# Optimization experiments

Hardware: AMD Instinct MI355X
Metric: run time of the kernel (lower is better)

The kernel has to match this reference:

```python
import jax, jax.numpy as jnp
import numpy as np

# Haar step along H (axis 1 of a (B,H,W) image): average / abs-diff of row pairs.
def _haar_y(img):
    odd, even = img[:, 0::2], img[:, 1::2]
    return (odd + even) / 2.0, jnp.abs(odd - even)

# Haar step along W (axis 2). In the original torch code this is done via
# permute + flip + Y-transform + permute + flip-back; the two flips act on the
# untouched H axis and cancel exactly, so the math reduces to pairing along W.
def _haar_x(img):
    odd, even = img[:, :, 0::2], img[:, :, 1::2]
    return (odd + even) / 2.0, jnp.abs(odd - even)

def _dwt2(img):  # (B,H,W) -> LL, LH, HL, HH each (B,H/2,W/2)
    L, H = _haar_y(img)
    LL, LH = _haar_x(L)
    HL, HH = _haar_x(H)
    return LL, LH, HL, HH

def setup_inputs() -> dict:
    key = jax.random.key(0)
    x = jax.random.uniform(key, (32, 3, 512, 512), dtype=jnp.float32)
    return {"x": x}

def reference(x):
    r, g, b = x[:, 0], x[:, 1], x[:, 2]
    # Level 1
    r1 = _dwt2(r); g1 = _dwt2(g); b1 = _dwt2(b)
    t1 = jnp.stack([*r1, *g1, *b1], axis=1)  # (B,12,H/2,W/2)
    # Level 2 (recursion on LL of each channel)
    r2 = _dwt2(r1[0]); g2 = _dwt2(g1[0]); b2 = _dwt2(b1[0])
    t2 = jnp.stack([*r2, *g2, *b2], axis=1)
    # Level 3
    r3 = _dwt2(r2[0]); g3 = _dwt2(g2[0]); b3 = _dwt2(b2[0])
    t3 = jnp.stack([*r3, *g3, *b3], axis=1)
    # Level 4 -- faithfully reproduces the original bug: the blue-channel
    # level-4 bands are computed from wavelet_L4/H4 left over from the green
    # channel, so b4 == g4.
    r4 = _dwt2(r3[0]); g4 = _dwt2(g3[0]); b4 = g4
    t4 = jnp.stack([*r4, *g4, *b4], axis=1)
    return (t1, t2, t3, t4)
```

## Files before the change

### kernel.cpp

```cpp
#include <hip/hip_runtime.h>

__global__ __launch_bounds__(256) void dwt_level_kernel(
    const float* __restrict__ src, float* __restrict__ dst,
    int W,
    int h, int shift,
    long src_b_stride, long src_c_stride,
    int nC, int dup)
{
    int pid = blockIdx.x * blockDim.x + threadIdx.x;
    int npix = h << shift;
    if (pid >= npix) return;

    int plane = blockIdx.y;
    int b = plane / nC;
    int c = plane - b * nC;

    int jw = pid & ((1 << shift) - 1);
    int i  = pid >> shift;

    const float* sp = src + (long)b * src_b_stride + (long)c * src_c_stride;
    const float4 r0 = *((const float4*)(sp + (long)(2 * i)     * W) + jw);
    const float4 r1 = *((const float4*)(sp + (long)(2 * i + 1) * W) + jw);

    float L00 = (r0.x + r1.x) * 0.5f;
    float L01 = (r0.y + r1.y) * 0.5f;
    float H00 = fabsf(r0.x - r1.x);
    float H01 = fabsf(r0.y - r1.y);
    float L10 = (r0.z + r1.z) * 0.5f;
    float L11 = (r0.w + r1.w) * 0.5f;
    float H10 = fabsf(r0.z - r1.z);
    float H11 = fabsf(r0.w - r1.w);

    float2 ll = make_float2((L00 + L01) * 0.5f, (L10 + L11) * 0.5f);
    float2 lh = make_float2(fabsf(L00 - L01), fabsf(L10 - L11));
    float2 hl = make_float2((H00 + H01) * 0.5f, (H10 + H11) * 0.5f);
    float2 hh = make_float2(fabsf(H00 - H01), fabsf(H10 - H11));

    int w = 2 << shift;
    long hw = (long)h * w;
    float* dp = dst + (long)(b * 12 + 4 * c) * hw + (long)i * w + 2 * jw;

    *(float2*)(dp + 0 * hw) = ll;
    *(float2*)(dp + 1 * hw) = lh;
    *(float2*)(dp + 2 * hw) = hl;
    *(float2*)(dp + 3 * hw) = hh;

    if (dup && c == nC - 1) {
        float* dp2 = dp + 4 * hw;
        *(float2*)(dp2 + 0 * hw) = ll;
        *(float2*)(dp2 + 1 * hw) = lh;
        *(float2*)(dp2 + 2 * hw) = hl;
        *(float2*)(dp2 + 3 * hw) = hh;
    }
}

extern "C" void kernel_launch(void* const* d_in, const int* in_sizes, int n_in,
                              void* d_out, int out_size, void* d_ws, size_t ws_size,
                              hipStream_t stream) {
    const float* x = (const float*)d_in[0];
    float* out = (float*)d_out;

    const long t1_off = 0;
    const long t2_off = t1_off + 32L * 12 * 256 * 256;
    const long t3_off = t2_off + 32L * 12 * 128 * 128;
    const long t4_off = t3_off + 32L * 12 * 64 * 64;

    dim3 blk(256);
    dwt_level_kernel<<<dim3(128, 96), blk, 0, stream>>>(
        x, out + t1_off, 512, 256, 7, 3L * 512 * 512, 512L * 512, 3, 0);
    dwt_level_kernel<<<dim3(32, 96), blk, 0, stream>>>(
        out + t1_off, out + t2_off, 256, 128, 6, 12L * 256 * 256, 4L * 256 * 256, 3, 0);
    dwt_level_kernel<<<dim3(8, 96), blk, 0, stream>>>(
        out + t2_off, out + t3_off, 128, 64, 5, 12L * 128 * 128, 4L * 128 * 128, 3, 0);
    dwt_level_kernel<<<dim3(2, 64), blk, 0, stream>>>(
        out + t3_off, out + t4_off, 64, 32, 4, 12L * 64 * 64, 4L * 64 * 64, 2, 1);
}
```

Before: 215.6 us.

## Fuse all four DWT levels into one kernel using shared-memory LL slabs

Replaces four per-level launches with a single kernel in which each block handles a 16-row slab of one input plane. The block computes all four decomposition levels, keeping each level's LL band in shared memory so deeper levels no longer re-read it from global memory. This removes three kernel launches and the global round-trips of the intermediate LL bands. In exchange it adds block-level barriers, and the later levels run with only a fraction of the block's threads active.

```diff
diff --git a/kernel.cpp b/kernel.cpp
--- a/kernel.cpp
+++ b/kernel.cpp
@@ -1,56 +1,122 @@
 #include <hip/hip_runtime.h>
 
-__global__ __launch_bounds__(256) void dwt_level_kernel(
-    const float* __restrict__ src, float* __restrict__ dst,
-    int W,
-    int h, int shift,
-    long src_b_stride, long src_c_stride,
-    int nC, int dup)
+
+__device__ __forceinline__ void haar2(const float4 r0, const float4 r1,
+                                      float2& ll, float2& lh,
+                                      float2& hl, float2& hh)
 {
-    int pid = blockIdx.x * blockDim.x + threadIdx.x;
-    int npix = h << shift;
-    if (pid >= npix) return;
+    float L0 = (r0.x + r1.x) * 0.5f;
+    float L1 = (r0.y + r1.y) * 0.5f;
+    float L2 = (r0.z + r1.z) * 0.5f;
+    float L3 = (r0.w + r1.w) * 0.5f;
+    float H0 = fabsf(r0.x - r1.x);
+    float H1 = fabsf(r0.y - r1.y);
+    float H2 = fabsf(r0.z - r1.z);
+    float H3 = fabsf(r0.w - r1.w);
+    ll = make_float2((L0 + L1) * 0.5f, (L2 + L3) * 0.5f);
+    lh = make_float2(fabsf(L0 - L1), fabsf(L2 - L3));
+    hl = make_float2((H0 + H1) * 0.5f, (H2 + H3) * 0.5f);
+    hh = make_float2(fabsf(H0 - H1), fabsf(H2 - H3));
+}
 
-    int plane = blockIdx.y;
-    int b = plane / nC;
-    int c = plane - b * nC;
+__global__ __launch_bounds__(256) void dwt_fused(
+    const float* __restrict__ src, float* __restrict__ out)
+{
+    __shared__ float ll1[8][256];
+    __shared__ float ll2[4][128];
+    __shared__ float ll3[2][64];
 
-    int jw = pid & ((1 << shift) - 1);
-    int i  = pid >> shift;
+    const int slab  = blockIdx.x;
+    const int plane = blockIdx.y;
+    const int b = plane / 3;
+    const int c = plane - 3 * b;
+    const int tid = threadIdx.x;
 
-    const float* sp = src + (long)b * src_b_stride + (long)c * src_c_stride;
-    const float4 r0 = *((const float4*)(sp + (long)(2 * i)     * W) + jw);
-    const float4 r1 = *((const float4*)(sp + (long)(2 * i + 1) * W) + jw);
+    const long t2_off = 32L * 12 * 256 * 256;
+    const long t3_off = t2_off + 32L * 12 * 128 * 128;
+    const long t4_off = t3_off + 32L * 12 * 64 * 64;
 
-    float L00 = (r0.x + r1.x) * 0.5f;
-    float L01 = (r0.y + r1.y) * 0.5f;
-    float H00 = fabsf(r0.x - r1.x);
-    float H01 = fabsf(r0.y - r1.y);
-    float L10 = (r0.z + r1.z) * 0.5f;
-    float L11 = (r0.w + r1.w) * 0.5f;
-    float H10 = fabsf(r0.z - r1.z);
-    float H11 = fabsf(r0.w - r1.w);
+    const float* sp = src + (long)plane * (512L * 512)
+                          + (long)slab * 16 * 512;
 
-    float2 ll = make_float2((L00 + L01) * 0.5f, (L10 + L11) * 0.5f);
-    float2 lh = make_float2(fabsf(L00 - L01), fabsf(L10 - L11));
-    float2 hl = make_float2((H00 + H01) * 0.5f, (H10 + H11) * 0.5f);
-    float2 hh = make_float2(fabsf(H00 - H01), fabsf(H10 - H11));
+    {
+        const long hw = 256L * 256;
+        float* dp_base = out + (long)(b * 12 + 4 * c) * hw;
+        #pragma unroll
+        for (int k = 0; k < 4; ++k) {
+            int pid = k * 256 + tid;
+            int i   = pid >> 7;
+            int jw  = pid & 127;
+            const float4 r0 = *((const float4*)(sp + (long)(2 * i)     * 512) + jw);
+            const float4 r1 = *((const float4*)(sp + (long)(2 * i + 1) * 512) + jw);
+            float2 ll, lh, hl, hh;
+            haar2(r0, r1, ll, lh, hl, hh);
+            float* dp = dp_base + (long)(slab * 8 + i) * 256 + 2 * jw;
+            *(float2*)(dp + 0 * hw) = ll;
+            *(float2*)(dp + 1 * hw) = lh;
+            *(float2*)(dp + 2 * hw) = hl;
+            *(float2*)(dp + 3 * hw) = hh;
+            *(float2*)&ll1[i][2 * jw] = ll;
+        }
+    }
+    __syncthreads();
 
-    int w = 2 << shift;
-    long hw = (long)h * w;
-    float* dp = dst + (long)(b * 12 + 4 * c) * hw + (long)i * w + 2 * jw;
+    {
+        int i  = tid >> 6;
+        int jw = tid & 63;
+        const float4 r0 = *((const float4*)&ll1[2 * i][4 * jw]);
+        const float4 r1 = *((const float4*)&ll1[2 * i + 1][4 * jw]);
+        float2 ll, lh, hl, hh;
+        haar2(r0, r1, ll, lh, hl, hh);
+        const long hw = 128L * 128;
+        float* dp = out + t2_off + (long)(b * 12 + 4 * c) * hw
+                        + (long)(slab * 4 + i) * 128 + 2 * jw;
+        *(float2*)(dp + 0 * hw) = ll;
+        *(float2*)(dp + 1 * hw) = lh;
+        *(float2*)(dp + 2 * hw) = hl;
+        *(float2*)(dp + 3 * hw) = hh;
+        *(float2*)&ll2[i][2 * jw] = ll;
+    }
+    __syncthreads();
 
-    *(float2*)(dp + 0 * hw) = ll;
-    *(float2*)(dp + 1 * hw) = lh;
-    *(float2*)(dp + 2 * hw) = hl;
-    *(float2*)(dp + 3 * hw) = hh;
+    if (tid < 64) {
+        int i  = tid >> 5;
+        int jw = tid & 31;
+        const float4 r0 = *((const float4*)&ll2[2 * i][4 * jw]);
+        const float4 r1 = *((const float4*)&ll2[2 * i + 1][4 * jw]);
+        float2 ll, lh, hl, hh;
+        haar2(r0, r1, ll, lh, hl, hh);
+        const long hw = 64L * 64;
+        float* dp = out + t3_off + (long)(b * 12 + 4 * c) * hw
+                        + (long)(slab * 2 + i) * 64 + 2 * jw;
+        *(float2*)(dp + 0 * hw) = ll;
+        *(float2*)(dp + 1 * hw) = lh;
+        *(float2*)(dp + 2 * hw) = hl;
+        *(float2*)(dp + 3 * hw) = hh;
+        *(float2*)&ll3[i][2 * jw] = ll;
+    }
+    __syncthreads();
 
-    if (dup && c == nC - 1) {
-        float* dp2 = dp + 4 * hw;
-        *(float2*)(dp2 + 0 * hw) = ll;
-        *(float2*)(dp2 + 1 * hw) = lh;
-        *(float2*)(dp2 + 2 * hw) = hl;
-        *(float2*)(dp2 + 3 * hw) = hh;
+    if (c < 2 && tid < 16) {
+        int jw = tid;
+        const float4 r0 = *((const float4*)&ll3[0][4 * jw]);
+        const float4 r1 = *((const float4*)&ll3[1][4 * jw]);
+        float2 ll, lh, hl, hh;
+        haar2(r0, r1, ll, lh, hl, hh);
+        const long hw = 32L * 32;
+        float* dp = out + t4_off + (long)(b * 12 + 4 * c) * hw
+                        + (long)slab * 32 + 2 * jw;
+        *(float2*)(dp + 0 * hw) = ll;
+        *(float2*)(dp + 1 * hw) = lh;
+        *(float2*)(dp + 2 * hw) = hl;
+        *(float2*)(dp + 3 * hw) = hh;
+        if (c == 1) {
+            float* dp2 = dp + 4 * hw;
+            *(float2*)(dp2 + 0 * hw) = ll;
+            *(float2*)(dp2 + 1 * hw) = lh;
+            *(float2*)(dp2 + 2 * hw) = hl;
+            *(float2*)(dp2 + 3 * hw) = hh;
+        }
     }
 }
 
@@ -59,19 +125,5 @@
                               hipStream_t stream) {
     const float* x = (const float*)d_in[0];
     float* out = (float*)d_out;
-
-    const long t1_off = 0;
-    const long t2_off = t1_off + 32L * 12 * 256 * 256;
-    const long t3_off = t2_off + 32L * 12 * 128 * 128;
-    const long t4_off = t3_off + 32L * 12 * 64 * 64;
-
-    dim3 blk(256);
-    dwt_level_kernel<<<dim3(128, 96), blk, 0, stream>>>(
-        x, out + t1_off, 512, 256, 7, 3L * 512 * 512, 512L * 512, 3, 0);
-    dwt_level_kernel<<<dim3(32, 96), blk, 0, stream>>>(
-        out + t1_off, out + t2_off, 256, 128, 6, 12L * 256 * 256, 4L * 256 * 256, 3, 0);
-    dwt_level_kernel<<<dim3(8, 96), blk, 0, stream>>>(
-        out + t2_off, out + t3_off, 128, 64, 5, 12L * 128 * 128, 4L * 128 * 128, 3, 0);
-    dwt_level_kernel<<<dim3(2, 64), blk, 0, stream>>>(
-        out + t3_off, out + t4_off, 64, 32, 4, 12L * 64 * 64, 4L * 64 * 64, 2, 1);
+    dwt_fused<<<dim3(32, 96), dim3(256), 0, stream>>>(x, out);
 }
```

Result: faster. 206.1 us (-4.4%).
